# Performance work log

Hardware: AMD Instinct MI355X
Metric: run time of the kernel (lower is better)

The kernel has to match this reference:

```python
import jax, jax.numpy as jnp
import numpy as np

N_NODES = 100000
N_EDGES = 1600000
D_FEAT = 64


def setup_inputs() -> dict:
    key = jax.random.key(0)
    k1, k2, k3 = jax.random.split(key, 3)
    embeddings = jax.random.normal(k1, (N_NODES, D_FEAT), dtype=jnp.float32)
    src = jax.random.randint(k2, (N_EDGES,), 0, N_NODES)
    dst = jax.random.randint(k3, (N_EDGES,), 0, N_NODES)
    return {"embeddings": embeddings, "src": src, "dst": dst, "n_nodes": N_NODES}


def reference(embeddings, src, dst, n_nodes):
    # SmoothFilter with norm='both': D^{-1/2} A D^{-1/2} X  (GCN propagation)
    ones = jnp.ones(src.shape[0], dtype=embeddings.dtype)
    out_deg = jnp.clip(jax.ops.segment_sum(ones, src, num_segments=n_nodes), 1.0)
    in_deg = jnp.clip(jax.ops.segment_sum(ones, dst, num_segments=n_nodes), 1.0)
    # pre-normalize by out-degree^{-1/2}
    h = embeddings * (out_deg ** -0.5)[:, None]          # [N, d]
    # copy_src + sum aggregation over edges (sparse neighbor sum)
    agg = jax.ops.segment_sum(h[src], dst, num_segments=n_nodes)  # [N, d]
    # post-normalize by in-degree^{-1/2}
    return agg * (in_deg ** -0.5)[:, None]
```

## Files before the change

### kernel.cpp

```cpp
#include <hip/hip_runtime.h>
#include <hip/hip_fp16.h>

#define D_FEAT 64
#define NPB 128
#define NBMAX 1024
#define CHUNK 4096
#define EPT 16
#define CAPB 2816
#define RPT 6

__global__ void zero_ints(int* __restrict__ p, int n) {
    int i = blockIdx.x * blockDim.x + threadIdx.x;
    int stride = gridDim.x * blockDim.x;
    for (int j = i; j < n; j += stride) p[j] = 0;
}

__global__ __launch_bounds__(256) void bcnt_kernel(
        const int* __restrict__ src, const int* __restrict__ dst, int n_edges,
        int* __restrict__ dbcnt8, int* __restrict__ sbcnt8) {
    __shared__ int ld[NBMAX];
    __shared__ int ls[NBMAX];
    int t = threadIdx.x;
    for (int i = t; i < NBMAX; i += 256) { ld[i] = 0; ls[i] = 0; }
    __syncthreads();
    int i0 = blockIdx.x * blockDim.x + t;
    int stride = gridDim.x * blockDim.x;
    for (int e = i0; e < n_edges; e += stride) {
        atomicAdd(&ld[dst[e] >> 7], 1);
        atomicAdd(&ls[src[e] >> 7], 1);
    }
    __syncthreads();
    int* dmy = dbcnt8 + (blockIdx.x & 7) * NBMAX;
    int* smy = sbcnt8 + (blockIdx.x & 7) * NBMAX;
    for (int i = t; i < NBMAX; i += 256) {
        if (ld[i]) atomicAdd(&dmy[i], ld[i]);
        if (ls[i]) atomicAdd(&smy[i], ls[i]);
    }
}

__global__ void scan2_kernel(const int* __restrict__ dbcnt8, const int* __restrict__ sbcnt8,
                             int* __restrict__ dbstart, int* __restrict__ gcursor,
                             int* __restrict__ sbstart, int* __restrict__ scursor,
                             int n_edges) {
    __shared__ int wsum[16];
    int t = threadIdx.x, lane = t & 63, w = t >> 6;
    const int* c8 = (blockIdx.x == 0) ? dbcnt8 : sbcnt8;
    int* bs = (blockIdx.x == 0) ? dbstart : sbstart;
    int* cur = (blockIdx.x == 0) ? gcursor : scursor;
    int v = 0;
    #pragma unroll
    for (int c = 0; c < 8; ++c) v += c8[c * NBMAX + t];
    int inc = v;
    #pragma unroll
    for (int off = 1; off < 64; off <<= 1) {
        int y = __shfl_up(inc, off);
        if (lane >= off) inc += y;
    }
    if (lane == 63) wsum[w] = inc;
    __syncthreads();
    int add = 0;
    #pragma unroll
    for (int i = 0; i < 15; ++i) if (i < w) add += wsum[i];
    int ex = add + inc - v;
    bs[t] = ex;
    cur[t] = ex;
    if (t == NBMAX - 1) bs[NBMAX] = n_edges;
}

__global__ __launch_bounds__(256) void dualpart_kernel(
        const int* __restrict__ src, const int* __restrict__ dst, int n_edges,
        int* __restrict__ gcursor, int* __restrict__ scursor,
        int* __restrict__ arrA, unsigned char* __restrict__ arrS) {
    __shared__ int lhist[NBMAX];
    __shared__ int lstart[NBMAX];
    __shared__ int ldelta[NBMAX];
    __shared__ int lcur[NBMAX];
    __shared__ int part[256];
    __shared__ int pkLDS[CHUNK];
    __shared__ unsigned short bktLDS[CHUNK];

    int t = threadIdx.x;
    long long cbase = (long long)blockIdx.x * CHUNK;
    int cnt = (n_edges - cbase < CHUNK) ? (int)(n_edges - cbase) : CHUNK;

    for (int i = t; i < NBMAX; i += 256) lhist[i] = 0;
    __syncthreads();

    int ssrc[EPT], sdst[EPT];
    #pragma unroll
    for (int i = 0; i < EPT; ++i) {
        long long e = cbase + t + i * 256;
        if (e < n_edges) {
            ssrc[i] = src[e];
            sdst[i] = dst[e];
            atomicAdd(&lhist[sdst[i] >> 7], 1);
        } else {
            ssrc[i] = -1;
            sdst[i] = -1;
        }
    }
    __syncthreads();

    int b0 = 4 * t;
    int h0 = lhist[b0], h1 = lhist[b0 + 1], h2v = lhist[b0 + 2], h3 = lhist[b0 + 3];
    int tot = h0 + h1 + h2v + h3;
    part[t] = tot;
    __syncthreads();
    for (int off = 1; off < 256; off <<= 1) {
        int x = (t >= off) ? part[t - off] : 0;
        __syncthreads();
        part[t] += x;
        __syncthreads();
    }
    int ex = part[t] - tot;
    lstart[b0] = ex;
    lstart[b0 + 1] = ex + h0;
    lstart[b0 + 2] = ex + h0 + h1;
    lstart[b0 + 3] = ex + h0 + h1 + h2v;
    __syncthreads();
    for (int b = t; b < NBMAX; b += 256) {
        lcur[b] = lstart[b];
        int c = lhist[b];
        if (c > 0) ldelta[b] = atomicAdd(&gcursor[b], c) - lstart[b];
    }
    __syncthreads();
    #pragma unroll
    for (int i = 0; i < EPT; ++i) {
        if (sdst[i] >= 0) {
            int b = sdst[i] >> 7;
            int slot = atomicAdd(&lcur[b], 1);
            pkLDS[slot] = (ssrc[i] << 7) | (sdst[i] & 127);
            bktLDS[slot] = (unsigned short)b;
        }
    }
    __syncthreads();
    for (int j = t; j < cnt; j += 256) {
        int b = bktLDS[j];
        arrA[j + ldelta[b]] = pkLDS[j];
    }
    __syncthreads();

    for (int i = t; i < NBMAX; i += 256) lhist[i] = 0;
    __syncthreads();
    #pragma unroll
    for (int i = 0; i < EPT; ++i) {
        if (ssrc[i] >= 0) atomicAdd(&lhist[ssrc[i] >> 7], 1);
    }
    __syncthreads();
    h0 = lhist[b0]; h1 = lhist[b0 + 1]; h2v = lhist[b0 + 2]; h3 = lhist[b0 + 3];
    tot = h0 + h1 + h2v + h3;
    part[t] = tot;
    __syncthreads();
    for (int off = 1; off < 256; off <<= 1) {
        int x = (t >= off) ? part[t - off] : 0;
        __syncthreads();
        part[t] += x;
        __syncthreads();
    }
    ex = part[t] - tot;
    lstart[b0] = ex;
    lstart[b0 + 1] = ex + h0;
    lstart[b0 + 2] = ex + h0 + h1;
    lstart[b0 + 3] = ex + h0 + h1 + h2v;
    __syncthreads();
    for (int b = t; b < NBMAX; b += 256) {
        lcur[b] = lstart[b];
        int c = lhist[b];
        if (c > 0) ldelta[b] = atomicAdd(&scursor[b], c) - lstart[b];
    }
    __syncthreads();
    unsigned char* stg = (unsigned char*)pkLDS;
    #pragma unroll
    for (int i = 0; i < EPT; ++i) {
        if (ssrc[i] >= 0) {
            int b = ssrc[i] >> 7;
            int slot = atomicAdd(&lcur[b], 1);
            stg[slot] = (unsigned char)(ssrc[i] & 127);
            bktLDS[slot] = (unsigned short)b;
        }
    }
    __syncthreads();
    for (int j = t; j < cnt; j += 256) {
        int b = bktLDS[j];
        arrS[j + ldelta[b]] = stg[j];
    }
}

__global__ __launch_bounds__(256) void prep_kernel(
        const float4* __restrict__ emb4, const unsigned char* __restrict__ arrS,
        const int* __restrict__ sbstart, uint2* __restrict__ h2, int n_nodes) {
    __shared__ int lh[NPB];
    __shared__ float lsc[NPB];
    int b = blockIdx.x, t = threadIdx.x;
    int s = sbstart[b], e = sbstart[b + 1];
    if (t < NPB) lh[t] = 0;
    __syncthreads();
    for (int i = s + t; i < e; i += 256) atomicAdd(&lh[arrS[i]], 1);
    __syncthreads();
    if (t < NPB) {
        int od = lh[t];
        lsc[t] = rsqrtf((float)(od > 1 ? od : 1));
    }
    __syncthreads();
    int nbase = b * NPB;
    int r = t >> 4, c = t & 15;
    for (int r0 = 0; r0 < NPB; r0 += 16) {
        int row = r0 + r;
        int node = nbase + row;
        if (node < n_nodes) {
            float sc = lsc[row];
            float4 v = emb4[(size_t)node * 16 + c];
            __half2 a = __floats2half2_rn(v.x * sc, v.y * sc);
            __half2 bb = __floats2half2_rn(v.z * sc, v.w * sc);
            union { __half2 h; unsigned int u; } ua, ub;
            ua.h = a; ub.h = bb;
            uint2 rr; rr.x = ua.u; rr.y = ub.u;
            h2[(size_t)node * 16 + c] = rr;
        }
    }
    if (b == 0 && t < 16) {
        uint2 z; z.x = 0; z.y = 0;
        h2[(size_t)n_nodes * 16 + t] = z;
    }
}

__global__ __launch_bounds__(512) void sortagg_kernel(
        const uint2* __restrict__ h2, const int* __restrict__ arrA,
        const int* __restrict__ dbstart, float* __restrict__ out, int n_nodes) {
    __shared__ int lh[NPB];
    __shared__ int lst[NPB];
    __shared__ int lcur[NPB];
    __shared__ int srcS[CAPB];
    int b = blockIdx.x, t = threadIdx.x;
    int s = dbstart[b], e = dbstart[b + 1];
    int cnt = e - s;
    bool fit = (cnt <= CAPB);

    if (t < NPB) lh[t] = 0;
    __syncthreads();
    int pkreg[RPT];
    if (fit) {
        #pragma unroll
        for (int i = 0; i < RPT; ++i) {
            int idx = t + i * 512;
            pkreg[i] = (idx < cnt) ? arrA[s + idx] : -1;
            if (pkreg[i] >= 0) atomicAdd(&lh[pkreg[i] & 127], 1);
        }
    } else {
        for (int i = t; i < cnt; i += 512) atomicAdd(&lh[arrA[s + i] & 127], 1);
    }
    __syncthreads();
    if (t < 64) {
        int l0 = lh[t], l1 = lh[t + 64];
        int a = l0;
        for (int off = 1; off < 64; off <<= 1) { int y = __shfl_up(a, off); if (t >= off) a += y; }
        int tot0 = __shfl(a, 63);
        int c = l1;
        for (int off = 1; off < 64; off <<= 1) { int y = __shfl_up(c, off); if (t >= off) c += y; }
        lst[t] = a - l0;
        lst[t + 64] = tot0 + c - l1;
    }
    __syncthreads();
    if (t < NPB) lcur[t] = lst[t];
    __syncthreads();
    if (fit) {
        #pragma unroll
        for (int i = 0; i < RPT; ++i) {
            if (pkreg[i] >= 0) {
                int slot = atomicAdd(&lcur[pkreg[i] & 127], 1);
                srcS[slot] = pkreg[i] >> 7;
            }
        }
    }
    __syncthreads();

    int w = t >> 6, L = t & 63, g = L >> 4, c = L & 15;
    int nbase = b * NPB;
    union { unsigned int u; __half2 h; } uc;
    for (int nl = w * 16; nl < w * 16 + 16; ++nl) {
        int node = nbase + nl;
        if (node >= n_nodes) break;
        int st = lst[nl];
        int deg = lh[nl];
        int en = st + deg;
        float ax = 0.f, ay = 0.f, az = 0.f, aw = 0.f;
        if (fit) {
            for (int eidx = st; eidx < en; eidx += 16) {
                int ea = eidx + g, eb = ea + 4, ec = ea + 8, ed = ea + 12;
                int sa = (ea < en) ? srcS[ea] : n_nodes;
                int sb = (eb < en) ? srcS[eb] : n_nodes;
                int sc = (ec < en) ? srcS[ec] : n_nodes;
                int sd = (ed < en) ? srcS[ed] : n_nodes;
                uint2 va = h2[(size_t)sa * 16 + c];
                uint2 vb = h2[(size_t)sb * 16 + c];
                uint2 vc = h2[(size_t)sc * 16 + c];
                uint2 vd = h2[(size_t)sd * 16 + c];
                float2 f;
                uc.u = va.x; f = __half22float2(uc.h); ax += f.x; ay += f.y;
                uc.u = va.y; f = __half22float2(uc.h); az += f.x; aw += f.y;
                uc.u = vb.x; f = __half22float2(uc.h); ax += f.x; ay += f.y;
                uc.u = vb.y; f = __half22float2(uc.h); az += f.x; aw += f.y;
                uc.u = vc.x; f = __half22float2(uc.h); ax += f.x; ay += f.y;
                uc.u = vc.y; f = __half22float2(uc.h); az += f.x; aw += f.y;
                uc.u = vd.x; f = __half22float2(uc.h); ax += f.x; ay += f.y;
                uc.u = vd.y; f = __half22float2(uc.h); az += f.x; aw += f.y;
            }
        } else {
            for (int i2 = g; i2 < cnt; i2 += 4) {
                int v = arrA[s + i2];
                if ((v & 127) == nl) {
                    int sa = v >> 7;
                    uint2 va = h2[(size_t)sa * 16 + c];
                    float2 f;
                    uc.u = va.x; f = __half22float2(uc.h); ax += f.x; ay += f.y;
                    uc.u = va.y; f = __half22float2(uc.h); az += f.x; aw += f.y;
                }
            }
        }
        ax += __shfl_xor(ax, 16); ay += __shfl_xor(ay, 16);
        az += __shfl_xor(az, 16); aw += __shfl_xor(aw, 16);
        ax += __shfl_xor(ax, 32); ay += __shfl_xor(ay, 32);
        az += __shfl_xor(az, 32); aw += __shfl_xor(aw, 32);
        if (g == 0) {
            float is = rsqrtf((float)(deg > 1 ? deg : 1));
            float4 r;
            r.x = ax * is; r.y = ay * is; r.z = az * is; r.w = aw * is;
            ((float4*)out)[(size_t)node * 16 + c] = r;
        }
    }
}

__global__ void fb_zero(float* __restrict__ out, long long n_out,
                        int* __restrict__ deg, int n_deg) {
    long long i = (long long)blockIdx.x * blockDim.x + threadIdx.x;
    long long stride = (long long)gridDim.x * blockDim.x;
    for (long long j = i; j < n_out; j += stride) out[j] = 0.0f;
    for (long long j = i; j < n_deg; j += stride) deg[j] = 0;
}

__global__ void fb_degree(const int* __restrict__ src, const int* __restrict__ dst,
                          int n_edges, int* __restrict__ outdeg, int* __restrict__ indeg) {
    int i = blockIdx.x * blockDim.x + threadIdx.x;
    int stride = gridDim.x * blockDim.x;
    for (int e = i; e < n_edges; e += stride) {
        atomicAdd(&outdeg[src[e]], 1);
        atomicAdd(&indeg[dst[e]], 1);
    }
}

__global__ void fb_scatter(const float* __restrict__ emb,
                           const int* __restrict__ src, const int* __restrict__ dst,
                           const int* __restrict__ outdeg,
                           float* __restrict__ out, int n_edges) {
    const int epb = blockDim.x >> 6;
    const int d = threadIdx.x & 63;
    long long e0 = (long long)blockIdx.x * epb + (threadIdx.x >> 6);
    long long estride = (long long)gridDim.x * epb;
    for (long long e = e0; e < n_edges; e += estride) {
        int s = src[e];
        int tt = dst[e];
        int od = outdeg[s];
        float v = emb[(long long)s * D_FEAT + d] * rsqrtf((float)(od > 1 ? od : 1));
        atomicAdd(&out[(long long)tt * D_FEAT + d], v);
    }
}

__global__ void fb_scale(float* __restrict__ out, const int* __restrict__ indeg,
                         long long n_elems) {
    long long i = (long long)blockIdx.x * blockDim.x + threadIdx.x;
    long long stride = (long long)gridDim.x * blockDim.x;
    for (long long j = i; j < n_elems; j += stride) {
        int id = indeg[(int)(j >> 6)];
        out[j] *= rsqrtf((float)(id > 1 ? id : 1));
    }
}

extern "C" void kernel_launch(void* const* d_in, const int* in_sizes, int n_in,
                              void* d_out, int out_size, void* d_ws, size_t ws_size,
                              hipStream_t stream) {
    const float* emb = (const float*)d_in[0];
    const int* src = (const int*)d_in[1];
    const int* dst = (const int*)d_in[2];
    const int n_nodes = in_sizes[0] / D_FEAT;
    const int n_edges = in_sizes[1];
    float* out = (float*)d_out;
    const int block = 256;
    const int nb = (n_nodes + NPB - 1) / NPB;
    const int K = NBMAX;

    int* dbcnt8 = (int*)d_ws;
    int* sbcnt8 = dbcnt8 + 8 * K;
    int* dbstart = sbcnt8 + 8 * K;
    int* gcursor = dbstart + K + 1;
    int* sbstart = gcursor + K;
    int* scursor = sbstart + K + 1;
    int* arrA = scursor + K;
    int* region = arrA + n_edges;
    unsigned char* arrS = (unsigned char*)region;
    uint2* h2 = (uint2*)region;

    size_t region_ints = (size_t)(n_nodes + 1) * 32;
    size_t arrS_ints = ((size_t)n_edges + 3) / 4;
    if (arrS_ints > region_ints) region_ints = arrS_ints;
    size_t need = (16 * (size_t)K + 2 * (size_t)(K + 1) + 2 * (size_t)K
                   + (size_t)n_edges + region_ints) * sizeof(int);

    if (ws_size >= need && nb <= K) {
        zero_ints<<<32, block, 0, stream>>>(dbcnt8, 16 * K);
        bcnt_kernel<<<384, block, 0, stream>>>(src, dst, n_edges, dbcnt8, sbcnt8);
        scan2_kernel<<<2, K, 0, stream>>>(dbcnt8, sbcnt8, dbstart, gcursor,
                                          sbstart, scursor, n_edges);
        int pblocks = (n_edges + CHUNK - 1) / CHUNK;
        dualpart_kernel<<<pblocks, 256, 0, stream>>>(src, dst, n_edges, gcursor,
                                                     scursor, arrA, arrS);
        prep_kernel<<<nb, 256, 0, stream>>>((const float4*)emb, arrS, sbstart,
                                            h2, n_nodes);
        sortagg_kernel<<<nb, 512, 0, stream>>>(h2, arrA, dbstart, out, n_nodes);
    } else {
        int* foutdeg = (int*)d_ws;
        int* findeg = foutdeg + n_nodes;
        long long n_out = (long long)n_nodes * D_FEAT;
        fb_zero<<<2048, block, 0, stream>>>(out, n_out, foutdeg, 2 * n_nodes);
        fb_degree<<<2048, block, 0, stream>>>(src, dst, n_edges, foutdeg, findeg);
        fb_scatter<<<2048, block, 0, stream>>>(emb, src, dst, foutdeg, out, n_edges);
        fb_scale<<<2048, block, 0, stream>>>(out, findeg, n_out);
    }
}
```

Baseline: 124.9 us.

## Coarsen source buckets to 512 nodes and split aggregation blocks per half bucket

Source-side out-degree bucketing now uses 256 buckets of 512 nodes with 16-bit local ids in place of 1024 buckets of 128 nodes. This shrinks the histogram, scan and scatter work in the partition kernel and lets prep run fewer, larger blocks. The sortagg kernel now launches two blocks per destination bucket, each handling 64 nodes, to double parallelism and cut per-block shared memory. In exchange every half-block reads the full bucket's edge list, and the source staging array doubles from 8-bit to 16-bit entries.

After: 127.2 us. About the same (+1.8%).

```diff
diff --git a/kernel.cpp b/kernel.cpp
--- a/kernel.cpp
+++ b/kernel.cpp
@@ -4,9 +4,13 @@
 #define D_FEAT 64
 #define NPB 128
 #define NBMAX 1024
+#define SBSH 9
+#define SNPB 512
+#define SBMAX 256
 #define CHUNK 4096
 #define EPT 16
 #define CAPB 2816
+#define CAPB_H 1536
 #define RPT 6
 
 __global__ void zero_ints(int* __restrict__ p, int n) {
@@ -19,23 +23,24 @@
         const int* __restrict__ src, const int* __restrict__ dst, int n_edges,
         int* __restrict__ dbcnt8, int* __restrict__ sbcnt8) {
     __shared__ int ld[NBMAX];
-    __shared__ int ls[NBMAX];
+    __shared__ int ls[SBMAX];
     int t = threadIdx.x;
-    for (int i = t; i < NBMAX; i += 256) { ld[i] = 0; ls[i] = 0; }
+    for (int i = t; i < NBMAX; i += 256) ld[i] = 0;
+    if (t < SBMAX) ls[t] = 0;
     __syncthreads();
     int i0 = blockIdx.x * blockDim.x + t;
     int stride = gridDim.x * blockDim.x;
     for (int e = i0; e < n_edges; e += stride) {
         atomicAdd(&ld[dst[e] >> 7], 1);
-        atomicAdd(&ls[src[e] >> 7], 1);
+        atomicAdd(&ls[src[e] >> SBSH], 1);
     }
     __syncthreads();
     int* dmy = dbcnt8 + (blockIdx.x & 7) * NBMAX;
-    int* smy = sbcnt8 + (blockIdx.x & 7) * NBMAX;
+    int* smy = sbcnt8 + (blockIdx.x & 7) * SBMAX;
     for (int i = t; i < NBMAX; i += 256) {
         if (ld[i]) atomicAdd(&dmy[i], ld[i]);
-        if (ls[i]) atomicAdd(&smy[i], ls[i]);
-    }
+    }
+    if (t < SBMAX && ls[t]) atomicAdd(&smy[t], ls[t]);
 }
 
 __global__ void scan2_kernel(const int* __restrict__ dbcnt8, const int* __restrict__ sbcnt8,
@@ -44,33 +49,55 @@
                              int n_edges) {
     __shared__ int wsum[16];
     int t = threadIdx.x, lane = t & 63, w = t >> 6;
-    const int* c8 = (blockIdx.x == 0) ? dbcnt8 : sbcnt8;
-    int* bs = (blockIdx.x == 0) ? dbstart : sbstart;
-    int* cur = (blockIdx.x == 0) ? gcursor : scursor;
-    int v = 0;
-    #pragma unroll
-    for (int c = 0; c < 8; ++c) v += c8[c * NBMAX + t];
-    int inc = v;
-    #pragma unroll
-    for (int off = 1; off < 64; off <<= 1) {
-        int y = __shfl_up(inc, off);
-        if (lane >= off) inc += y;
-    }
-    if (lane == 63) wsum[w] = inc;
-    __syncthreads();
-    int add = 0;
-    #pragma unroll
-    for (int i = 0; i < 15; ++i) if (i < w) add += wsum[i];
-    int ex = add + inc - v;
-    bs[t] = ex;
-    cur[t] = ex;
-    if (t == NBMAX - 1) bs[NBMAX] = n_edges;
+    if (blockIdx.x == 0) {
+        int v = 0;
+        #pragma unroll
+        for (int c = 0; c < 8; ++c) v += dbcnt8[c * NBMAX + t];
+        int inc = v;
+        #pragma unroll
+        for (int off = 1; off < 64; off <<= 1) {
+            int y = __shfl_up(inc, off);
+            if (lane >= off) inc += y;
+        }
+        if (lane == 63) wsum[w] = inc;
+        __syncthreads();
+        int add = 0;
+        #pragma unroll
+        for (int i = 0; i < 15; ++i) if (i < w) add += wsum[i];
+        int ex = add + inc - v;
+        dbstart[t] = ex;
+        gcursor[t] = ex;
+        if (t == NBMAX - 1) dbstart[NBMAX] = n_edges;
+    } else {
+        int v = 0, inc = 0;
+        if (t < SBMAX) {
+            #pragma unroll
+            for (int c = 0; c < 8; ++c) v += sbcnt8[c * SBMAX + t];
+            inc = v;
+            #pragma unroll
+            for (int off = 1; off < 64; off <<= 1) {
+                int y = __shfl_up(inc, off);
+                if (lane >= off) inc += y;
+            }
+            if (lane == 63) wsum[w] = inc;
+        }
+        __syncthreads();
+        if (t < SBMAX) {
+            int add = 0;
+            #pragma unroll
+            for (int i = 0; i < 3; ++i) if (i < w) add += wsum[i];
+            int ex = add + inc - v;
+            sbstart[t] = ex;
+            scursor[t] = ex;
+            if (t == SBMAX - 1) sbstart[SBMAX] = n_edges;
+        }
+    }
 }
 
 __global__ __launch_bounds__(256) void dualpart_kernel(
         const int* __restrict__ src, const int* __restrict__ dst, int n_edges,
         int* __restrict__ gcursor, int* __restrict__ scursor,
-        int* __restrict__ arrA, unsigned char* __restrict__ arrS) {
+        int* __restrict__ arrA, unsigned short* __restrict__ arrS16) {
     __shared__ int lhist[NBMAX];
     __shared__ int lstart[NBMAX];
     __shared__ int ldelta[NBMAX];
@@ -140,16 +167,15 @@
     }
     __syncthreads();
 
-    for (int i = t; i < NBMAX; i += 256) lhist[i] = 0;
+    if (t < SBMAX) lhist[t] = 0;
     __syncthreads();
     #pragma unroll
     for (int i = 0; i < EPT; ++i) {
-        if (ssrc[i] >= 0) atomicAdd(&lhist[ssrc[i] >> 7], 1);
-    }
-    __syncthreads();
-    h0 = lhist[b0]; h1 = lhist[b0 + 1]; h2v = lhist[b0 + 2]; h3 = lhist[b0 + 3];
-    tot = h0 + h1 + h2v + h3;
-    part[t] = tot;
+        if (ssrc[i] >= 0) atomicAdd(&lhist[ssrc[i] >> SBSH], 1);
+    }
+    __syncthreads();
+    int h = lhist[t];
+    part[t] = h;
     __syncthreads();
     for (int off = 1; off < 256; off <<= 1) {
         int x = (t >= off) ? part[t - off] : 0;
@@ -157,54 +183,46 @@
         part[t] += x;
         __syncthreads();
     }
-    ex = part[t] - tot;
-    lstart[b0] = ex;
-    lstart[b0 + 1] = ex + h0;
-    lstart[b0 + 2] = ex + h0 + h1;
-    lstart[b0 + 3] = ex + h0 + h1 + h2v;
-    __syncthreads();
-    for (int b = t; b < NBMAX; b += 256) {
-        lcur[b] = lstart[b];
-        int c = lhist[b];
-        if (c > 0) ldelta[b] = atomicAdd(&scursor[b], c) - lstart[b];
-    }
-    __syncthreads();
-    unsigned char* stg = (unsigned char*)pkLDS;
+    ex = part[t] - h;
+    lcur[t] = ex;
+    if (h > 0) ldelta[t] = atomicAdd(&scursor[t], h) - ex;
+    __syncthreads();
+    unsigned short* stg = (unsigned short*)pkLDS;
     #pragma unroll
     for (int i = 0; i < EPT; ++i) {
         if (ssrc[i] >= 0) {
-            int b = ssrc[i] >> 7;
+            int b = ssrc[i] >> SBSH;
             int slot = atomicAdd(&lcur[b], 1);
-            stg[slot] = (unsigned char)(ssrc[i] & 127);
+            stg[slot] = (unsigned short)(ssrc[i] & (SNPB - 1));
             bktLDS[slot] = (unsigned short)b;
         }
     }
     __syncthreads();
     for (int j = t; j < cnt; j += 256) {
         int b = bktLDS[j];
-        arrS[j + ldelta[b]] = stg[j];
+        arrS16[j + ldelta[b]] = stg[j];
     }
 }
 
 __global__ __launch_bounds__(256) void prep_kernel(
-        const float4* __restrict__ emb4, const unsigned char* __restrict__ arrS,
+        const float4* __restrict__ emb4, const unsigned short* __restrict__ arrS16,
         const int* __restrict__ sbstart, uint2* __restrict__ h2, int n_nodes) {
-    __shared__ int lh[NPB];
-    __shared__ float lsc[NPB];
+    __shared__ int lh[SNPB];
+    __shared__ float lsc[SNPB];
     int b = blockIdx.x, t = threadIdx.x;
     int s = sbstart[b], e = sbstart[b + 1];
-    if (t < NPB) lh[t] = 0;
-    __syncthreads();
-    for (int i = s + t; i < e; i += 256) atomicAdd(&lh[arrS[i]], 1);
-    __syncthreads();
-    if (t < NPB) {
-        int od = lh[t];
-        lsc[t] = rsqrtf((float)(od > 1 ? od : 1));
-    }
-    __syncthreads();
-    int nbase = b * NPB;
+    for (int i = t; i < SNPB; i += 256) lh[i] = 0;
+    __syncthreads();
+    for (int i = s + t; i < e; i += 256) atomicAdd(&lh[arrS16[i]], 1);
+    __syncthreads();
+    for (int i = t; i < SNPB; i += 256) {
+        int od = lh[i];
+        lsc[i] = rsqrtf((float)(od > 1 ? od : 1));
+    }
+    __syncthreads();
+    int nbase = b * SNPB;
     int r = t >> 4, c = t & 15;
-    for (int r0 = 0; r0 < NPB; r0 += 16) {
+    for (int r0 = 0; r0 < SNPB; r0 += 16) {
         int row = r0 + r;
         int node = nbase + row;
         if (node < n_nodes) {
@@ -227,64 +245,71 @@
 __global__ __launch_bounds__(512) void sortagg_kernel(
         const uint2* __restrict__ h2, const int* __restrict__ arrA,
         const int* __restrict__ dbstart, float* __restrict__ out, int n_nodes) {
-    __shared__ int lh[NPB];
-    __shared__ int lst[NPB];
-    __shared__ int lcur[NPB];
-    __shared__ int srcS[CAPB];
-    int b = blockIdx.x, t = threadIdx.x;
+    __shared__ int lh[64];
+    __shared__ int lst[64];
+    __shared__ int lcur[64];
+    __shared__ int srcS[CAPB_H];
+    int b = blockIdx.x >> 1, half = blockIdx.x & 1;
+    int t = threadIdx.x;
     int s = dbstart[b], e = dbstart[b + 1];
     int cnt = e - s;
     bool fit = (cnt <= CAPB);
 
-    if (t < NPB) lh[t] = 0;
+    if (t < 64) lh[t] = 0;
     __syncthreads();
     int pkreg[RPT];
     if (fit) {
         #pragma unroll
         for (int i = 0; i < RPT; ++i) {
             int idx = t + i * 512;
-            pkreg[i] = (idx < cnt) ? arrA[s + idx] : -1;
-            if (pkreg[i] >= 0) atomicAdd(&lh[pkreg[i] & 127], 1);
+            int pk = (idx < cnt) ? arrA[s + idx] : -1;
+            pkreg[i] = pk;
+            if (pk >= 0 && (((pk >> 6) & 1) == half)) atomicAdd(&lh[pk & 63], 1);
         }
     } else {
-        for (int i = t; i < cnt; i += 512) atomicAdd(&lh[arrA[s + i] & 127], 1);
+        for (int i = t; i < cnt; i += 512) {
+            int v = arrA[s + i];
+            if (((v >> 6) & 1) == half) atomicAdd(&lh[v & 63], 1);
+        }
     }
     __syncthreads();
     if (t < 64) {
-        int l0 = lh[t], l1 = lh[t + 64];
+        int l0 = lh[t];
         int a = l0;
-        for (int off = 1; off < 64; off <<= 1) { int y = __shfl_up(a, off); if (t >= off) a += y; }
-        int tot0 = __shfl(a, 63);
-        int c = l1;
-        for (int off = 1; off < 64; off <<= 1) { int y = __shfl_up(c, off); if (t >= off) c += y; }
+        #pragma unroll
+        for (int off = 1; off < 64; off <<= 1) {
+            int y = __shfl_up(a, off);
+            if (t >= off) a += y;
+        }
         lst[t] = a - l0;
-        lst[t + 64] = tot0 + c - l1;
-    }
-    __syncthreads();
-    if (t < NPB) lcur[t] = lst[t];
-    __syncthreads();
-    if (fit) {
+        lcur[t] = a - l0;
+    }
+    __syncthreads();
+    int halfcnt = lst[63] + lh[63];
+    bool useS = fit && (halfcnt <= CAPB_H);
+    if (useS) {
         #pragma unroll
         for (int i = 0; i < RPT; ++i) {
-            if (pkreg[i] >= 0) {
-                int slot = atomicAdd(&lcur[pkreg[i] & 127], 1);
-                srcS[slot] = pkreg[i] >> 7;
+            int pk = pkreg[i];
+            if (pk >= 0 && (((pk >> 6) & 1) == half)) {
+                int slot = atomicAdd(&lcur[pk & 63], 1);
+                srcS[slot] = pk >> 7;
             }
         }
     }
     __syncthreads();
 
     int w = t >> 6, L = t & 63, g = L >> 4, c = L & 15;
-    int nbase = b * NPB;
+    int nbase = b * NPB + half * 64;
     union { unsigned int u; __half2 h; } uc;
-    for (int nl = w * 16; nl < w * 16 + 16; ++nl) {
+    for (int nl = w * 8; nl < w * 8 + 8; ++nl) {
         int node = nbase + nl;
         if (node >= n_nodes) break;
         int st = lst[nl];
         int deg = lh[nl];
         int en = st + deg;
         float ax = 0.f, ay = 0.f, az = 0.f, aw = 0.f;
-        if (fit) {
+        if (useS) {
             for (int eidx = st; eidx < en; eidx += 16) {
                 int ea = eidx + g, eb = ea + 4, ec = ea + 8, ed = ea + 12;
                 int sa = (ea < en) ? srcS[ea] : n_nodes;
@@ -306,9 +331,10 @@
                 uc.u = vd.y; f = __half22float2(uc.h); az += f.x; aw += f.y;
             }
         } else {
+            int hv = (half << 6) | nl;
             for (int i2 = g; i2 < cnt; i2 += 4) {
                 int v = arrA[s + i2];
-                if ((v & 127) == nl) {
+                if ((v & 127) == hv) {
                     int sa = v >> 7;
                     uint2 va = h2[(size_t)sa * 16 + c];
                     float2 f;
@@ -386,36 +412,37 @@
     float* out = (float*)d_out;
     const int block = 256;
     const int nb = (n_nodes + NPB - 1) / NPB;
+    const int nb2 = (n_nodes + SNPB - 1) / SNPB;
     const int K = NBMAX;
 
     int* dbcnt8 = (int*)d_ws;
     int* sbcnt8 = dbcnt8 + 8 * K;
-    int* dbstart = sbcnt8 + 8 * K;
+    int* dbstart = sbcnt8 + 8 * SBMAX;
     int* gcursor = dbstart + K + 1;
     int* sbstart = gcursor + K;
-    int* scursor = sbstart + K + 1;
-    int* arrA = scursor + K;
+    int* scursor = sbstart + SBMAX + 1;
+    int* arrA = scursor + SBMAX;
     int* region = arrA + n_edges;
-    unsigned char* arrS = (unsigned char*)region;
+    unsigned short* arrS16 = (unsigned short*)region;
     uint2* h2 = (uint2*)region;
 
     size_t region_ints = (size_t)(n_nodes + 1) * 32;
-    size_t arrS_ints = ((size_t)n_edges + 3) / 4;
+    size_t arrS_ints = ((size_t)n_edges + 1) / 2;
     if (arrS_ints > region_ints) region_ints = arrS_ints;
-    size_t need = (16 * (size_t)K + 2 * (size_t)(K + 1) + 2 * (size_t)K
+    size_t need = (8 * (size_t)K + 8 * SBMAX + (K + 1) + K + (SBMAX + 1) + SBMAX
                    + (size_t)n_edges + region_ints) * sizeof(int);
 
-    if (ws_size >= need && nb <= K) {
-        zero_ints<<<32, block, 0, stream>>>(dbcnt8, 16 * K);
+    if (ws_size >= need && nb <= K && nb2 <= SBMAX) {
+        zero_ints<<<32, block, 0, stream>>>(dbcnt8, 8 * K + 8 * SBMAX);
         bcnt_kernel<<<384, block, 0, stream>>>(src, dst, n_edges, dbcnt8, sbcnt8);
         scan2_kernel<<<2, K, 0, stream>>>(dbcnt8, sbcnt8, dbstart, gcursor,
                                           sbstart, scursor, n_edges);
         int pblocks = (n_edges + CHUNK - 1) / CHUNK;
         dualpart_kernel<<<pblocks, 256, 0, stream>>>(src, dst, n_edges, gcursor,
-                                                     scursor, arrA, arrS);
-        prep_kernel<<<nb, 256, 0, stream>>>((const float4*)emb, arrS, sbstart,
-                                            h2, n_nodes);
-        sortagg_kernel<<<nb, 512, 0, stream>>>(h2, arrA, dbstart, out, n_nodes);
+                                                     scursor, arrA, arrS16);
+        prep_kernel<<<nb2, 256, 0, stream>>>((const float4*)emb, arrS16, sbstart,
+                                             h2, n_nodes);
+        sortagg_kernel<<<2 * nb, 512, 0, stream>>>(h2, arrA, dbstart, out, n_nodes);
     } else {
         int* foutdeg = (int*)d_ws;
         int* findeg = foutdeg + n_nodes;
```

## Split each destination bucket across two blocks in aggregation kernel

Applied to the files above, without the earlier changes.

The aggregation kernel now launches two blocks per 128-node destination bucket, each handling 64 nodes. Both blocks read the bucket's full edge list but each keeps only its half. This doubles the grid to improve occupancy and load balance and shrinks shared memory per block. In exchange, each bucket's edge list is read and filtered twice, and per-wave work drops to 8 nodes.

After: 121.5 us. 2.7% less time.

```diff
diff --git a/kernel.cpp b/kernel.cpp
--- a/kernel.cpp
+++ b/kernel.cpp
@@ -7,6 +7,7 @@
 #define CHUNK 4096
 #define EPT 16
 #define CAPB 2816
+#define CAPB_H 1536
 #define RPT 6
 
 __global__ void zero_ints(int* __restrict__ p, int n) {
@@ -227,64 +228,71 @@
 __global__ __launch_bounds__(512) void sortagg_kernel(
         const uint2* __restrict__ h2, const int* __restrict__ arrA,
         const int* __restrict__ dbstart, float* __restrict__ out, int n_nodes) {
-    __shared__ int lh[NPB];
-    __shared__ int lst[NPB];
-    __shared__ int lcur[NPB];
-    __shared__ int srcS[CAPB];
-    int b = blockIdx.x, t = threadIdx.x;
+    __shared__ int lh[64];
+    __shared__ int lst[64];
+    __shared__ int lcur[64];
+    __shared__ int srcS[CAPB_H];
+    int b = blockIdx.x >> 1, half = blockIdx.x & 1;
+    int t = threadIdx.x;
     int s = dbstart[b], e = dbstart[b + 1];
     int cnt = e - s;
     bool fit = (cnt <= CAPB);
 
-    if (t < NPB) lh[t] = 0;
+    if (t < 64) lh[t] = 0;
     __syncthreads();
     int pkreg[RPT];
     if (fit) {
         #pragma unroll
         for (int i = 0; i < RPT; ++i) {
             int idx = t + i * 512;
-            pkreg[i] = (idx < cnt) ? arrA[s + idx] : -1;
-            if (pkreg[i] >= 0) atomicAdd(&lh[pkreg[i] & 127], 1);
+            int pk = (idx < cnt) ? arrA[s + idx] : -1;
+            pkreg[i] = pk;
+            if (pk >= 0 && (((pk >> 6) & 1) == half)) atomicAdd(&lh[pk & 63], 1);
         }
     } else {
-        for (int i = t; i < cnt; i += 512) atomicAdd(&lh[arrA[s + i] & 127], 1);
+        for (int i = t; i < cnt; i += 512) {
+            int v = arrA[s + i];
+            if (((v >> 6) & 1) == half) atomicAdd(&lh[v & 63], 1);
+        }
     }
     __syncthreads();
     if (t < 64) {
-        int l0 = lh[t], l1 = lh[t + 64];
+        int l0 = lh[t];
         int a = l0;
-        for (int off = 1; off < 64; off <<= 1) { int y = __shfl_up(a, off); if (t >= off) a += y; }
-        int tot0 = __shfl(a, 63);
-        int c = l1;
-        for (int off = 1; off < 64; off <<= 1) { int y = __shfl_up(c, off); if (t >= off) c += y; }
+        #pragma unroll
+        for (int off = 1; off < 64; off <<= 1) {
+            int y = __shfl_up(a, off);
+            if (t >= off) a += y;
+        }
         lst[t] = a - l0;
-        lst[t + 64] = tot0 + c - l1;
-    }
-    __syncthreads();
-    if (t < NPB) lcur[t] = lst[t];
-    __syncthreads();
-    if (fit) {
+        lcur[t] = a - l0;
+    }
+    __syncthreads();
+    int halfcnt = lst[63] + lh[63];
+    bool useS = fit && (halfcnt <= CAPB_H);
+    if (useS) {
         #pragma unroll
         for (int i = 0; i < RPT; ++i) {
-            if (pkreg[i] >= 0) {
-                int slot = atomicAdd(&lcur[pkreg[i] & 127], 1);
-                srcS[slot] = pkreg[i] >> 7;
+            int pk = pkreg[i];
+            if (pk >= 0 && (((pk >> 6) & 1) == half)) {
+                int slot = atomicAdd(&lcur[pk & 63], 1);
+                srcS[slot] = pk >> 7;
             }
         }
     }
     __syncthreads();
 
     int w = t >> 6, L = t & 63, g = L >> 4, c = L & 15;
-    int nbase = b * NPB;
+    int nbase = b * NPB + half * 64;
     union { unsigned int u; __half2 h; } uc;
-    for (int nl = w * 16; nl < w * 16 + 16; ++nl) {
+    for (int nl = w * 8; nl < w * 8 + 8; ++nl) {
         int node = nbase + nl;
         if (node >= n_nodes) break;
         int st = lst[nl];
         int deg = lh[nl];
         int en = st + deg;
         float ax = 0.f, ay = 0.f, az = 0.f, aw = 0.f;
-        if (fit) {
+        if (useS) {
             for (int eidx = st; eidx < en; eidx += 16) {
                 int ea = eidx + g, eb = ea + 4, ec = ea + 8, ed = ea + 12;
                 int sa = (ea < en) ? srcS[ea] : n_nodes;
@@ -306,9 +314,10 @@
                 uc.u = vd.y; f = __half22float2(uc.h); az += f.x; aw += f.y;
             }
         } else {
+            int hv = (half << 6) | nl;
             for (int i2 = g; i2 < cnt; i2 += 4) {
                 int v = arrA[s + i2];
-                if ((v & 127) == nl) {
+                if ((v & 127) == hv) {
                     int sa = v >> 7;
                     uint2 va = h2[(size_t)sa * 16 + c];
                     float2 f;
@@ -415,7 +424,7 @@
                                                      scursor, arrA, arrS);
         prep_kernel<<<nb, 256, 0, stream>>>((const float4*)emb, arrS, sbstart,
                                             h2, n_nodes);
-        sortagg_kernel<<<nb, 512, 0, stream>>>(h2, arrA, dbstart, out, n_nodes);
+        sortagg_kernel<<<2 * nb, 512, 0, stream>>>(h2, arrA, dbstart, out, n_nodes);
     } else {
         int* foutdeg = (int*)d_ws;
         int* findeg = foutdeg + n_nodes;
```
